# Kernel tuning notes

Measured on AMD Instinct MI355X. Metric: run time of the kernel, lower is better.

The kernel has to match this reference:

```python
import jax, jax.numpy as jnp
import numpy as np

D_MODEL = 1024
NUM_HEADS = 16
D_K = D_MODEL // NUM_HEADS
B, S = 2, 2048


def setup_inputs() -> dict:
    key = jax.random.key(0)
    ks = jax.random.split(key, 11)
    lim = 1.0 / np.sqrt(D_MODEL)  # torch Linear default init range
    def lin(kw, kb):
        W = jax.random.uniform(kw, (D_MODEL, D_MODEL), jnp.float32, -lim, lim)
        b = jax.random.uniform(kb, (D_MODEL,), jnp.float32, -lim, lim)
        return W, b
    Wq, bq = lin(ks[0], ks[1])
    Wk, bk = lin(ks[2], ks[3])
    Wv, bv = lin(ks[4], ks[5])
    Wo, bo = lin(ks[6], ks[7])
    return {
        "Q": jax.random.normal(ks[8], (B, S, D_MODEL), jnp.float32),
        "K": jax.random.normal(ks[9], (B, S, D_MODEL), jnp.float32),
        "V": jax.random.normal(ks[10], (B, S, D_MODEL), jnp.float32),
        "Wq": Wq, "bq": bq, "Wk": Wk, "bk": bk,
        "Wv": Wv, "bv": bv, "Wo": Wo, "bo": bo,
        "validate": False,
    }


def _split_heads(x):
    b, s, _ = x.shape
    return x.reshape(b, s, NUM_HEADS, D_K).transpose(0, 2, 1, 3)  # [B,H,S,Dk]


def reference(Q, K, V, Wq, bq, Wk, bk, Wv, bv, Wo, bo, validate):
    # Linear projections (torch Linear: x @ W.T + b)
    q = _split_heads(Q @ Wq.T + bq)
    k = _split_heads(K @ Wk.T + bk)
    v = _split_heads(V @ Wv.T + bv)
    scale = 1.0 / jnp.sqrt(jnp.asarray(D_K, q.dtype))
    scores = jnp.einsum("bhqd,bhkd->bhqk", q, k) * scale  # [B,H,S,S]
    attn = jax.nn.softmax(scores, axis=-1)
    out = jnp.einsum("bhqk,bhkd->bhqd", attn, v)  # [B,H,S,Dk]
    out = out.transpose(0, 2, 1, 3).reshape(Q.shape[0], Q.shape[1], D_MODEL)
    return out @ Wo.T + bo
```

## Files before the change

### kernel.cpp

```cpp
#include <hip/hip_runtime.h>


typedef short bf16x8 __attribute__((ext_vector_type(8)));
typedef float f32x4 __attribute__((ext_vector_type(4)));

#define D_MODEL 1024
#define NHEAD 16
#define DK 64
#define BB 2
#define SS 2048
#define MROWS (BB * SS)
#define C1 0.18033688011112042f

__device__ __forceinline__ unsigned short f2bf(float f) {
  unsigned u = __builtin_bit_cast(unsigned, f);
  u += 0x7fffu + ((u >> 16) & 1u);
  return (unsigned short)(u >> 16);
}
__device__ __forceinline__ unsigned pack2(float a, float b) {
  return (unsigned)f2bf(a) | ((unsigned)f2bf(b) << 16);
}
__device__ __forceinline__ unsigned cvtpk(float lo, float hi) {
  unsigned r;
  asm("v_cvt_pk_bf16_f32 %0, %1, %2" : "=v"(r) : "v"(lo), "v"(hi));
  return r;
}
__device__ __forceinline__ float max3f(float a, float b, float c) {
  float d;
  asm("v_max3_f32 %0, %1, %2, %3" : "=v"(d) : "v"(a), "v"(b), "v"(c));
  return d;
}

typedef __attribute__((address_space(3))) unsigned int as3u;
typedef const __attribute__((address_space(1))) unsigned int as1u;
__device__ __forceinline__ void gload16(void* lds, const void* g) {
  __builtin_amdgcn_global_load_lds((as1u*)g, (as3u*)lds, 16, 0, 0);
}

struct CvtArgs {
  const float* s[7];
  unsigned short* d[7];
  int n8[7];
};

__global__ __launch_bounds__(256) void convert_bf16(CvtArgs a) {
  const int slot = blockIdx.y;
  const float* __restrict__ s = a.s[slot];
  unsigned short* __restrict__ d = a.d[slot];
  const int n8 = a.n8[slot];
  for (int i = blockIdx.x * 256 + threadIdx.x; i < n8; i += gridDim.x * 256) {
    const size_t off = (size_t)i * 8;
    const float4 v0 = *(const float4*)&s[off];
    const float4 v1 = *(const float4*)&s[off + 4];
    uint4 p;
    p.x = pack2(v0.x, v0.y); p.y = pack2(v0.z, v0.w);
    p.z = pack2(v1.x, v1.y); p.w = pack2(v1.z, v1.w);
    *(uint4*)&d[off] = p;
  }
}

template <int MODE>
__device__ __forceinline__ void gemm128(unsigned short* smem,
                                        const unsigned short* __restrict__ A,
                                        const unsigned short* __restrict__ B,
                                        const float* __restrict__ bias,
                                        float scale, int bm, int nb,
                                        float* __restrict__ Cf,
                                        unsigned short* __restrict__ Cb) {
  unsigned short* As = smem;
  unsigned short* Bs = smem + 128 * 64;
  const int tid = threadIdx.x;
  const int lane = tid & 63, w = tid >> 6;
  const int wm = w >> 1, wn = w & 1;
  const int l15 = lane & 15, l4 = lane >> 4;

  f32x4 acc[4][4];
#pragma unroll
  for (int m = 0; m < 4; ++m)
#pragma unroll
    for (int n = 0; n < 4; ++n) acc[m][n] = (f32x4){0.f, 0.f, 0.f, 0.f};

  for (int k0 = 0; k0 < D_MODEL; k0 += 64) {
    __syncthreads();
#pragma unroll
    for (int i = 0; i < 4; ++i) {
      const int flat = i * 256 + tid;
      const int row = flat >> 3, g = flat & 7;
      const int gs = (g ^ (row & 7)) << 3;
      gload16(&As[flat * 8], &A[(size_t)(bm * 128 + row) * D_MODEL + k0 + gs]);
    }
#pragma unroll
    for (int i = 0; i < 4; ++i) {
      const int flat = i * 256 + tid;
      const int row = flat >> 3, g = flat & 7;
      const int gs = (g ^ (row & 7)) << 3;
      gload16(&Bs[flat * 8], &B[(size_t)(nb * 128 + row) * D_MODEL + k0 + gs]);
    }
    __syncthreads();
#pragma unroll
    for (int kk = 0; kk < 2; ++kk) {
      bf16x8 af[4], bf[4];
#pragma unroll
      for (int m = 0; m < 4; ++m) {
        const int r = wm * 64 + m * 16 + l15;
        af[m] = *(const bf16x8*)&As[r * 64 + (((kk * 4 + l4) ^ (r & 7)) << 3)];
      }
#pragma unroll
      for (int n = 0; n < 4; ++n) {
        const int r = wn * 64 + n * 16 + l15;
        bf[n] = *(const bf16x8*)&Bs[r * 64 + (((kk * 4 + l4) ^ (r & 7)) << 3)];
      }
#pragma unroll
      for (int m = 0; m < 4; ++m)
#pragma unroll
        for (int n = 0; n < 4; ++n)
          acc[m][n] = __builtin_amdgcn_mfma_f32_16x16x32_bf16(af[m], bf[n], acc[m][n], 0, 0, 0);
    }
  }

  if (MODE != 2) {
#pragma unroll
    for (int m = 0; m < 4; ++m)
#pragma unroll
      for (int n = 0; n < 4; ++n) {
        const int col = nb * 128 + wn * 64 + n * 16 + l15;
        const float bv = bias[col];
#pragma unroll
        for (int r = 0; r < 4; ++r) {
          const int row = bm * 128 + wm * 64 + m * 16 + l4 * 4 + r;
          const float v = (acc[m][n][r] + bv) * scale;
          if (MODE == 0) Cb[(size_t)row * D_MODEL + col] = f2bf(v);
          else           Cf[(size_t)row * D_MODEL + col] = v;
        }
      }
  } else {
    unsigned short* T = smem;
    __syncthreads();
#pragma unroll
    for (int m = 0; m < 4; ++m)
#pragma unroll
      for (int n = 0; n < 4; ++n) {
        const int cl = wn * 64 + n * 16 + l15;
        const float bv = bias[nb * 128 + cl];
#pragma unroll
        for (int r = 0; r < 4; ++r) {
          const int rl = wm * 64 + m * 16 + l4 * 4 + r;
          const int byte = cl * 256 + ((((rl >> 3) ^ (cl & 7))) << 4) + ((rl & 7) << 1);
          *(unsigned short*)((char*)T + byte) = f2bf(acc[m][n][r] + bv);
        }
      }
    __syncthreads();
#pragma unroll
    for (int c = 0; c < 8; ++c) {
      const int chunk = c * 256 + tid;
      const int cl = chunk >> 4, rl0 = (chunk & 15) * 8;
      const int byte = cl * 256 + (((rl0 >> 3) ^ (cl & 7)) << 4);
      const uint4 val = *(const uint4*)((const char*)T + byte);
      const int gcol = nb * 128 + cl;
      const int bb = (bm * 128) >> 11;
      const int s = ((bm * 128) & 2047) + rl0;
      *(uint4*)&Cb[(size_t)(bb * 1024 + gcol) * SS + s] = val;
    }
  }
}

__global__ __launch_bounds__(256, 3) void gemm_qkv(
    const unsigned short* __restrict__ Xq, const unsigned short* __restrict__ Xk,
    const unsigned short* __restrict__ Xv,
    const unsigned short* __restrict__ Wq, const float* __restrict__ bq,
    const unsigned short* __restrict__ Wk, const float* __restrict__ bk,
    const unsigned short* __restrict__ Wv, const float* __restrict__ bv,
    unsigned short* __restrict__ q, unsigned short* __restrict__ k,
    unsigned short* __restrict__ vT) {
  __shared__ __align__(16) unsigned short smem[2 * 128 * 64];
  const int bn = blockIdx.x, bm = blockIdx.y;
  const int z = bn >> 3, nb = bn & 7;
  if (z == 0) {
    gemm128<0>(smem, Xq, Wq, bq, C1, bm, nb, nullptr, q);
  } else if (z == 1) {
    gemm128<0>(smem, Xk, Wk, bk, 1.0f, bm, nb, nullptr, k);
  } else {
    gemm128<2>(smem, Xv, Wv, bv, 1.0f, bm, nb, nullptr, vT);
  }
}

__global__ __launch_bounds__(256, 3) void gemm_o(const unsigned short* __restrict__ A,
                                                 const unsigned short* __restrict__ W,
                                                 const float* __restrict__ bi,
                                                 float* __restrict__ out) {
  __shared__ __align__(16) unsigned short smem[2 * 128 * 64];
  gemm128<1>(smem, A, W, bi, 1.0f, blockIdx.y, blockIdx.x, out, nullptr);
}

__global__ __launch_bounds__(256, 2) void attn_kernel(
    const unsigned short* __restrict__ Qp, const unsigned short* __restrict__ Kp,
    const unsigned short* __restrict__ vTp, unsigned short* __restrict__ Op) {
  __shared__ __align__(16) unsigned short Kt[2][64 * 64];
  __shared__ __align__(16) unsigned short Vt[2][64 * 64];
  __shared__ __align__(16) unsigned short Pt[4][32 * 64];
  const int tid = threadIdx.x;
  const int lane = tid & 63, w = tid >> 6;
  const int l15 = lane & 15, l4 = lane >> 4;
  const int bh = blockIdx.x;
  const int b = bh >> 4, h = bh & 15;
  const int qb = blockIdx.y;
  const size_t baseQ = (size_t)b * SS * D_MODEL + (size_t)h * DK;
  const size_t baseV = (size_t)(b * 1024 + h * 64) * SS;

  bf16x8 aq[2][2];
#pragma unroll
  for (int m = 0; m < 2; ++m) {
    const int qrow = qb * 128 + w * 32 + m * 16 + l15;
#pragma unroll
    for (int kk = 0; kk < 2; ++kk)
      aq[m][kk] = *(const bf16x8*)&Qp[baseQ + (size_t)qrow * D_MODEL + kk * 32 + l4 * 8];
  }

  const bf16x8 vone = {0x3F80, 0x3F80, 0x3F80, 0x3F80, 0x3F80, 0x3F80, 0x3F80, 0x3F80};

  float rm[2] = {-1e30f, -1e30f};
  f32x4 acc[2][5];
#pragma unroll
  for (int m = 0; m < 2; ++m)
#pragma unroll
    for (int d = 0; d < 5; ++d) acc[m][d] = (f32x4){0.f, 0.f, 0.f, 0.f};

  auto stage = [&](int buf, int kt) {
#pragma unroll
    for (int i = 0; i < 2; ++i) {
      const int flat = (w * 2 + i) * 64 + lane;
      const int row = flat >> 3, g = flat & 7;
      gload16(&Kt[buf][flat * 8],
              &Kp[baseQ + (size_t)(kt * 64 + row) * D_MODEL + ((g ^ (row & 7)) << 3)]);
    }
#pragma unroll
    for (int i = 0; i < 2; ++i) {
      const int flat = (w * 2 + i) * 64 + lane;
      const int row = flat >> 3, g = flat & 7;
      gload16(&Vt[buf][flat * 8],
              &vTp[baseV + (size_t)row * SS + kt * 64 + ((g ^ (row & 7)) << 3)]);
    }
  };

  stage(0, 0);
  __syncthreads();
  int cur = 0;
  for (int kt = 0; kt < SS / 64; ++kt) {
    if (kt + 1 < SS / 64) stage(cur ^ 1, kt + 1);

    f32x4 st[2][4];
#pragma unroll
    for (int m = 0; m < 2; ++m)
#pragma unroll
      for (int n = 0; n < 4; ++n) st[m][n] = (f32x4){0.f, 0.f, 0.f, 0.f};
#pragma unroll
    for (int kk = 0; kk < 2; ++kk) {
      bf16x8 kf[4];
#pragma unroll
      for (int n = 0; n < 4; ++n) {
        const int r = n * 16 + l15;
        kf[n] = *(const bf16x8*)&Kt[cur][r * 64 + (((kk * 4 + l4) ^ (r & 7)) << 3)];
      }
      __builtin_amdgcn_s_setprio(1);
#pragma unroll
      for (int m = 0; m < 2; ++m)
#pragma unroll
        for (int n = 0; n < 4; ++n)
          st[m][n] = __builtin_amdgcn_mfma_f32_16x16x32_bf16(kf[n], aq[m][kk], st[m][n], 0, 0, 0);
      __builtin_amdgcn_s_setprio(0);
    }

    float mx[2];
#pragma unroll
    for (int m = 0; m < 2; ++m) {
      const float a0 = max3f(st[m][0][0], st[m][0][1], st[m][0][2]);
      const float a1 = max3f(st[m][0][3], st[m][1][0], st[m][1][1]);
      const float a2 = max3f(st[m][1][2], st[m][1][3], st[m][2][0]);
      const float a3 = max3f(st[m][2][1], st[m][2][2], st[m][2][3]);
      const float a4 = max3f(st[m][3][0], st[m][3][1], st[m][3][2]);
      float v = fmaxf(max3f(a0, a1, a2), max3f(a3, a4, st[m][3][3]));
      v = fmaxf(v, __shfl_xor(v, 16));
      v = fmaxf(v, __shfl_xor(v, 32));
      mx[m] = v;
    }
    if (__any((mx[0] > rm[0] + 8.f) | (mx[1] > rm[1] + 8.f))) {
#pragma unroll
      for (int m = 0; m < 2; ++m) {
        const float nm = fmaxf(rm[m], mx[m]);
        const float alpha = exp2f(rm[m] - nm);
        rm[m] = nm;
#pragma unroll
        for (int r = 0; r < 4; ++r) {
          const float ar = __shfl(alpha, l4 * 4 + r);
#pragma unroll
          for (int d = 0; d < 5; ++d) acc[m][d][r] *= ar;
        }
      }
    }
#pragma unroll
    for (int m = 0; m < 2; ++m)
#pragma unroll
      for (int n = 0; n < 4; ++n)
#pragma unroll
        for (int r = 0; r < 4; ++r) st[m][n][r] = exp2f(st[m][n][r] - rm[m]);

#pragma unroll
    for (int m = 0; m < 2; ++m)
#pragma unroll
      for (int n = 0; n < 4; ++n)
#pragma unroll
        for (int c = 0; c < 2; ++c) {
          const int col = n * 16 + l4 * 4 + 2 * c;
          const int row = m * 16 + l15;
          const int sw = (((col >> 3) ^ (row & 7)) << 3) + (col & 7);
          *(unsigned*)&Pt[w][row * 64 + sw] = cvtpk(st[m][n][2 * c], st[m][n][2 * c + 1]);
        }

#pragma unroll
    for (int kk = 0; kk < 2; ++kk) {
      bf16x8 ap[2], vf[4];
#pragma unroll
      for (int m = 0; m < 2; ++m) {
        const int r = m * 16 + l15;
        ap[m] = *(const bf16x8*)&Pt[w][r * 64 + (((kk * 4 + l4) ^ (r & 7)) << 3)];
      }
#pragma unroll
      for (int d = 0; d < 4; ++d) {
        const int r = d * 16 + l15;
        vf[d] = *(const bf16x8*)&Vt[cur][r * 64 + (((kk * 4 + l4) ^ (r & 7)) << 3)];
      }
      __builtin_amdgcn_s_setprio(1);
#pragma unroll
      for (int m = 0; m < 2; ++m) {
#pragma unroll
        for (int d = 0; d < 4; ++d)
          acc[m][d] = __builtin_amdgcn_mfma_f32_16x16x32_bf16(ap[m], vf[d], acc[m][d], 0, 0, 0);
        acc[m][4] = __builtin_amdgcn_mfma_f32_16x16x32_bf16(ap[m], vone, acc[m][4], 0, 0, 0);
      }
      __builtin_amdgcn_s_setprio(0);
    }

    __syncthreads();
    cur ^= 1;
  }

#pragma unroll
  for (int m = 0; m < 2; ++m) {
    float inv[4];
#pragma unroll
    for (int r = 0; r < 4; ++r) inv[r] = 1.0f / acc[m][4][r];
#pragma unroll
    for (int d = 0; d < 4; ++d)
#pragma unroll
      for (int r = 0; r < 4; ++r) {
        const int orow = qb * 128 + w * 32 + m * 16 + l4 * 4 + r;
        Op[baseQ + (size_t)orow * D_MODEL + d * 16 + l15] = f2bf(acc[m][d][r] * inv[r]);
      }
  }
}

extern "C" void kernel_launch(void* const* d_in, const int* in_sizes, int n_in,
                              void* d_out, int out_size, void* d_ws, size_t ws_size,
                              hipStream_t stream) {
  const float* Qin = (const float*)d_in[0];
  const float* Kin = (const float*)d_in[1];
  const float* Vin = (const float*)d_in[2];
  const float* Wq = (const float*)d_in[3];
  const float* bq = (const float*)d_in[4];
  const float* Wk = (const float*)d_in[5];
  const float* bk = (const float*)d_in[6];
  const float* Wv = (const float*)d_in[7];
  const float* bv = (const float*)d_in[8];
  const float* Wo = (const float*)d_in[9];
  const float* bo = (const float*)d_in[10];
  float* out = (float*)d_out;

  const size_t NX = (size_t)MROWS * D_MODEL;
  const size_t NW = (size_t)D_MODEL * D_MODEL;
  unsigned short* ws = (unsigned short*)d_ws;
  unsigned short* q  = ws;
  unsigned short* k  = ws + NX;
  unsigned short* vT = ws + 2 * NX;
  unsigned short* Xq = ws + 3 * NX;
  unsigned short* Xk = ws + 4 * NX;
  unsigned short* Xv = ws + 5 * NX;
  unsigned short* wq = ws + 6 * NX;
  unsigned short* wk = wq + NW;
  unsigned short* wv = wk + NW;
  unsigned short* wo = wv + NW;
  unsigned short* ao = Xq;

  CvtArgs ca;
  ca.s[0] = Qin; ca.d[0] = Xq; ca.n8[0] = (int)(NX / 8);
  ca.s[1] = Kin; ca.d[1] = Xk; ca.n8[1] = (int)(NX / 8);
  ca.s[2] = Vin; ca.d[2] = Xv; ca.n8[2] = (int)(NX / 8);
  ca.s[3] = Wq;  ca.d[3] = wq; ca.n8[3] = (int)(NW / 8);
  ca.s[4] = Wk;  ca.d[4] = wk; ca.n8[4] = (int)(NW / 8);
  ca.s[5] = Wv;  ca.d[5] = wv; ca.n8[5] = (int)(NW / 8);
  ca.s[6] = Wo;  ca.d[6] = wo; ca.n8[6] = (int)(NW / 8);
  convert_bf16<<<dim3(1024, 7), 256, 0, stream>>>(ca);

  gemm_qkv<<<dim3(24, 32), 256, 0, stream>>>(
      Xq, Xk, Xv, wq, bq, wk, bk, wv, bv, q, k, vT);
  attn_kernel<<<dim3(BB * NHEAD, SS / 128), 256, 0, stream>>>(q, k, vT, ao);
  gemm_o<<<dim3(8, 32), 256, 0, stream>>>(ao, wo, bo, out);
}
```

Before: 249.9 us.

## Triple-buffer LDS with vmcnt waits in GEMMs and attention, swizzle block order

Switches the projection GEMMs and the attention kernel from single- or double-buffered LDS staging to a three-slot ring. Loads for tile t+2 are issued before tile t is computed, and explicit s_waitcnt vmcnt counts plus raw barriers replace __syncthreads. The GEMM kernels also remap block indices into a grouped order to improve L2 reuse, and launch bounds drop to one block per SM because LDS use triples. The attention kernel also loses its setprio hints. The cost is lower occupancy and fragile hand-counted vmcnt values that must match the number of outstanding loads.

```diff
diff --git a/kernel.cpp b/kernel.cpp
--- a/kernel.cpp
+++ b/kernel.cpp
@@ -36,6 +36,10 @@
 __device__ __forceinline__ void gload16(void* lds, const void* g) {
   __builtin_amdgcn_global_load_lds((as1u*)g, (as3u*)lds, 16, 0, 0);
 }
+__device__ __forceinline__ void waitv16() { asm volatile("s_waitcnt vmcnt(16)" ::: "memory"); }
+__device__ __forceinline__ void waitv8()  { asm volatile("s_waitcnt vmcnt(8)"  ::: "memory"); }
+__device__ __forceinline__ void waitv4()  { asm volatile("s_waitcnt vmcnt(4)"  ::: "memory"); }
+__device__ __forceinline__ void waitv0()  { asm volatile("s_waitcnt vmcnt(0)"  ::: "memory"); }
 
 struct CvtArgs {
   const float* s[7];
@@ -67,21 +71,15 @@
                                         float scale, int bm, int nb,
                                         float* __restrict__ Cf,
                                         unsigned short* __restrict__ Cb) {
-  unsigned short* As = smem;
-  unsigned short* Bs = smem + 128 * 64;
+  const int BUF = 2 * 128 * 64;
   const int tid = threadIdx.x;
   const int lane = tid & 63, w = tid >> 6;
   const int wm = w >> 1, wn = w & 1;
   const int l15 = lane & 15, l4 = lane >> 4;
 
-  f32x4 acc[4][4];
-#pragma unroll
-  for (int m = 0; m < 4; ++m)
-#pragma unroll
-    for (int n = 0; n < 4; ++n) acc[m][n] = (f32x4){0.f, 0.f, 0.f, 0.f};
-
-  for (int k0 = 0; k0 < D_MODEL; k0 += 64) {
-    __syncthreads();
+  auto stage = [&](int slot, int k0) {
+    unsigned short* As = smem + slot * BUF;
+    unsigned short* Bs = As + 128 * 64;
 #pragma unroll
     for (int i = 0; i < 4; ++i) {
       const int flat = i * 256 + tid;
@@ -96,7 +94,25 @@
       const int gs = (g ^ (row & 7)) << 3;
       gload16(&Bs[flat * 8], &B[(size_t)(nb * 128 + row) * D_MODEL + k0 + gs]);
     }
-    __syncthreads();
+  };
+
+  f32x4 acc[4][4];
+#pragma unroll
+  for (int m = 0; m < 4; ++m)
+#pragma unroll
+    for (int n = 0; n < 4; ++n) acc[m][n] = (f32x4){0.f, 0.f, 0.f, 0.f};
+
+  stage(0, 0);
+  stage(1, 64);
+#pragma unroll
+  for (int t = 0; t < 16; ++t) {
+    if (t + 2 < 16) stage((t + 2) % 3, (t + 2) * 64);
+    if (t < 14) waitv16();
+    else if (t == 14) waitv8();
+    else waitv0();
+    __builtin_amdgcn_s_barrier();
+    unsigned short* As = smem + (t % 3) * BUF;
+    unsigned short* Bs = As + 128 * 64;
 #pragma unroll
     for (int kk = 0; kk < 2; ++kk) {
       bf16x8 af[4], bf[4];
@@ -116,6 +132,7 @@
         for (int n = 0; n < 4; ++n)
           acc[m][n] = __builtin_amdgcn_mfma_f32_16x16x32_bf16(af[m], bf[n], acc[m][n], 0, 0, 0);
     }
+    __builtin_amdgcn_s_barrier();
   }
 
   if (MODE != 2) {
@@ -135,7 +152,6 @@
       }
   } else {
     unsigned short* T = smem;
-    __syncthreads();
 #pragma unroll
     for (int m = 0; m < 4; ++m)
 #pragma unroll
@@ -164,7 +180,7 @@
   }
 }
 
-__global__ __launch_bounds__(256, 3) void gemm_qkv(
+__global__ __launch_bounds__(256, 1) void gemm_qkv(
     const unsigned short* __restrict__ Xq, const unsigned short* __restrict__ Xk,
     const unsigned short* __restrict__ Xv,
     const unsigned short* __restrict__ Wq, const float* __restrict__ bq,
@@ -172,31 +188,38 @@
     const unsigned short* __restrict__ Wv, const float* __restrict__ bv,
     unsigned short* __restrict__ q, unsigned short* __restrict__ k,
     unsigned short* __restrict__ vT) {
-  __shared__ __align__(16) unsigned short smem[2 * 128 * 64];
-  const int bn = blockIdx.x, bm = blockIdx.y;
+  __shared__ __align__(16) unsigned short smem[3 * 2 * 128 * 64];
+  const int lin = blockIdx.x + 24 * blockIdx.y;
+  const int swz = (lin % 8) * 96 + lin / 8;
+  const int bn = swz % 24, bm = swz / 24;
   const int z = bn >> 3, nb = bn & 7;
-  if (z == 0) {
-    gemm128<0>(smem, Xq, Wq, bq, C1, bm, nb, nullptr, q);
-  } else if (z == 1) {
-    gemm128<0>(smem, Xk, Wk, bk, 1.0f, bm, nb, nullptr, k);
+  if (z < 2) {
+    const unsigned short* X = z ? Xk : Xq;
+    const unsigned short* W = z ? Wk : Wq;
+    const float* bi = z ? bk : bq;
+    unsigned short* O = z ? k : q;
+    gemm128<0>(smem, X, W, bi, z ? 1.0f : C1, bm, nb, nullptr, O);
   } else {
     gemm128<2>(smem, Xv, Wv, bv, 1.0f, bm, nb, nullptr, vT);
   }
 }
 
-__global__ __launch_bounds__(256, 3) void gemm_o(const unsigned short* __restrict__ A,
+__global__ __launch_bounds__(256, 1) void gemm_o(const unsigned short* __restrict__ A,
                                                  const unsigned short* __restrict__ W,
                                                  const float* __restrict__ bi,
                                                  float* __restrict__ out) {
-  __shared__ __align__(16) unsigned short smem[2 * 128 * 64];
-  gemm128<1>(smem, A, W, bi, 1.0f, blockIdx.y, blockIdx.x, out, nullptr);
+  __shared__ __align__(16) unsigned short smem[3 * 2 * 128 * 64];
+  const int lin = blockIdx.x + 8 * blockIdx.y;
+  const int swz = (lin % 8) * 32 + lin / 8;
+  const int bn = swz % 8, bm = swz / 8;
+  gemm128<1>(smem, A, W, bi, 1.0f, bm, bn, out, nullptr);
 }
 
 __global__ __launch_bounds__(256, 2) void attn_kernel(
     const unsigned short* __restrict__ Qp, const unsigned short* __restrict__ Kp,
     const unsigned short* __restrict__ vTp, unsigned short* __restrict__ Op) {
-  __shared__ __align__(16) unsigned short Kt[2][64 * 64];
-  __shared__ __align__(16) unsigned short Vt[2][64 * 64];
+  __shared__ __align__(16) unsigned short Kt[3][64 * 64];
+  __shared__ __align__(16) unsigned short Vt[3][64 * 64];
   __shared__ __align__(16) unsigned short Pt[4][32 * 64];
   const int tid = threadIdx.x;
   const int lane = tid & 63, w = tid >> 6;
@@ -243,10 +266,18 @@
   };
 
   stage(0, 0);
-  __syncthreads();
-  int cur = 0;
+  stage(1, 1);
+#pragma unroll 1
   for (int kt = 0; kt < SS / 64; ++kt) {
-    if (kt + 1 < SS / 64) stage(cur ^ 1, kt + 1);
+    const int bs = kt % 3;
+    if (kt < SS / 64 - 2) {
+      int bst = bs + 2; if (bst >= 3) bst -= 3;
+      stage(bst, kt + 2);
+    }
+    if (kt < SS / 64 - 2) waitv8();
+    else if (kt == SS / 64 - 2) waitv4();
+    else waitv0();
+    __builtin_amdgcn_s_barrier();
 
     f32x4 st[2][4];
 #pragma unroll
@@ -259,15 +290,13 @@
 #pragma unroll
       for (int n = 0; n < 4; ++n) {
         const int r = n * 16 + l15;
-        kf[n] = *(const bf16x8*)&Kt[cur][r * 64 + (((kk * 4 + l4) ^ (r & 7)) << 3)];
-      }
-      __builtin_amdgcn_s_setprio(1);
+        kf[n] = *(const bf16x8*)&Kt[bs][r * 64 + (((kk * 4 + l4) ^ (r & 7)) << 3)];
+      }
 #pragma unroll
       for (int m = 0; m < 2; ++m)
 #pragma unroll
         for (int n = 0; n < 4; ++n)
           st[m][n] = __builtin_amdgcn_mfma_f32_16x16x32_bf16(kf[n], aq[m][kk], st[m][n], 0, 0, 0);
-      __builtin_amdgcn_s_setprio(0);
     }
 
     float mx[2];
@@ -327,9 +356,8 @@
 #pragma unroll
       for (int d = 0; d < 4; ++d) {
         const int r = d * 16 + l15;
-        vf[d] = *(const bf16x8*)&Vt[cur][r * 64 + (((kk * 4 + l4) ^ (r & 7)) << 3)];
-      }
-      __builtin_amdgcn_s_setprio(1);
+        vf[d] = *(const bf16x8*)&Vt[bs][r * 64 + (((kk * 4 + l4) ^ (r & 7)) << 3)];
+      }
 #pragma unroll
       for (int m = 0; m < 2; ++m) {
 #pragma unroll
@@ -337,11 +365,9 @@
           acc[m][d] = __builtin_amdgcn_mfma_f32_16x16x32_bf16(ap[m], vf[d], acc[m][d], 0, 0, 0);
         acc[m][4] = __builtin_amdgcn_mfma_f32_16x16x32_bf16(ap[m], vone, acc[m][4], 0, 0, 0);
       }
-      __builtin_amdgcn_s_setprio(0);
-    }
-
-    __syncthreads();
-    cur ^= 1;
+    }
+
+    __builtin_amdgcn_s_barrier();
   }
 
 #pragma unroll
```

New measurement: 237.3 us. -5.0%, faster.
